# Kernel tuning notes

Hardware: AMD Instinct MI355X
Metric: run time of the kernel (lower is better)

The kernel has to match this reference:

```python
import jax, jax.numpy as jnp
import numpy as np

N_NODES = 50000
N_EDGES = 800000
N_GRAPHS = 512
VOCAB = 100000
EMB = 64
HID = 128
CLASSES = 2


def setup_inputs() -> dict:
    key = jax.random.key(0)
    ks = jax.random.split(key, 12)
    x = jax.random.randint(ks[0], (N_NODES,), 0, VOCAB)
    edge_index = jax.random.randint(ks[1], (2, N_EDGES), 0, N_NODES)
    batch = jnp.sort(jax.random.randint(ks[2], (N_NODES,), 0, N_GRAPHS))
    s = lambda fan_in: 1.0 / np.sqrt(fan_in)
    emb_table = jax.random.normal(ks[3], (VOCAB, EMB), jnp.float32)
    w1_l = jax.random.uniform(ks[4], (EMB, HID), jnp.float32, -s(EMB), s(EMB))
    b1 = jnp.zeros((HID,), jnp.float32)
    w1_r = jax.random.uniform(ks[5], (EMB, HID), jnp.float32, -s(EMB), s(EMB))
    w2_l = jax.random.uniform(ks[6], (HID, HID), jnp.float32, -s(HID), s(HID))
    b2 = jnp.zeros((HID,), jnp.float32)
    w2_r = jax.random.uniform(ks[7], (HID, HID), jnp.float32, -s(HID), s(HID))
    w_out = jax.random.uniform(ks[8], (HID, CLASSES), jnp.float32, -s(HID), s(HID))
    b_out = jnp.zeros((CLASSES,), jnp.float32)
    return {"x": x, "edge_index": edge_index, "batch": batch,
            "emb_table": emb_table, "w1_l": w1_l, "b1": b1, "w1_r": w1_r,
            "w2_l": w2_l, "b2": b2, "w2_r": w2_r, "w_out": w_out, "b_out": b_out}


def _sage_conv(h, src, dst, w_l, b_l, w_r):
    # PyG SAGEConv (mean aggr): out = lin_l(mean_{j in N(i)} x_j) + lin_r(x_i)
    msg = h[src]                                              # [E, F] gather
    agg = jax.ops.segment_sum(msg, dst, num_segments=N_NODES)  # [N, F]
    deg = jax.ops.segment_sum(jnp.ones((src.shape[0],), h.dtype), dst,
                              num_segments=N_NODES)
    mean = agg / jnp.maximum(deg, 1.0)[:, None]
    return mean @ w_l + b_l + h @ w_r


def reference(x, edge_index, batch, emb_table, w1_l, b1, w1_r,
              w2_l, b2, w2_r, w_out, b_out):
    src, dst = edge_index[0], edge_index[1]
    h = emb_table[x]                                          # [N, EMB]
    h = jax.nn.relu(_sage_conv(h, src, dst, w1_l, b1, w1_r))
    # dropout is identity in eval mode
    h = jax.nn.relu(_sage_conv(h, src, dst, w2_l, b2, w2_r))
    # global mean pool over graphs
    pooled = jax.ops.segment_sum(h, batch, num_segments=N_GRAPHS)
    cnt = jax.ops.segment_sum(jnp.ones((N_NODES,), h.dtype), batch,
                              num_segments=N_GRAPHS)
    pooled = pooled / jnp.maximum(cnt, 1.0)[:, None]
    return pooled @ w_out + b_out                              # [G, CLASSES]
```

## Files before the change

### kernel.cpp

```cpp
#include <hip/hip_runtime.h>
#include <hip/hip_bf16.h>

#define N_NODES 50000
#define N_EDGES 800000
#define N_GRAPHS 512
#define EMB 64
#define HID 128

__global__ void k_embed_hist(const int* __restrict__ x, const float* __restrict__ emb,
                             const int* __restrict__ ei, float* __restrict__ h0,
                             int* __restrict__ deg) {
    int t = blockIdx.x * 256 + threadIdx.x;
    if (t >= N_EDGES) return;
    int n = t >> 4, c4 = t & 15;
    const float4* e4 = (const float4*)emb;
    ((float4*)h0)[(size_t)n * 16 + c4] = e4[(size_t)x[n] * 16 + c4];
    atomicAdd(&deg[ei[N_EDGES + t]], 1);
}

__global__ void k_scanA(const int* __restrict__ deg, int* __restrict__ rowptr,
                        int* __restrict__ bsums) {
    __shared__ int s[256];
    int t = threadIdx.x, i = blockIdx.x * 256 + t;
    int v = (i < N_NODES) ? deg[i] : 0;
    s[t] = v; __syncthreads();
    int xv = v;
    for (int off = 1; off < 256; off <<= 1) {
        int y = (t >= off) ? s[t - off] : 0;
        __syncthreads();
        xv += y; s[t] = xv;
        __syncthreads();
    }
    if (i < N_NODES) rowptr[i] = xv - v;
    if (t == 255) bsums[blockIdx.x] = xv;
}

__global__ void k_scanB(int* __restrict__ bsums, int nb) {
    __shared__ int s[256];
    int t = threadIdx.x;
    int v = (t < nb) ? bsums[t] : 0;
    s[t] = v; __syncthreads();
    int xv = v;
    for (int off = 1; off < 256; off <<= 1) {
        int y = (t >= off) ? s[t - off] : 0;
        __syncthreads();
        xv += y; s[t] = xv;
        __syncthreads();
    }
    if (t < nb) bsums[t] = xv - v;
}

__global__ void k_scanC(int* __restrict__ rowptr, int* __restrict__ wp,
                        const int* __restrict__ bsums) {
    int i = blockIdx.x * 256 + threadIdx.x;
    if (i < N_NODES) {
        int v = rowptr[i] + bsums[blockIdx.x];
        rowptr[i] = v;
        wp[i] = v;
    }
    if (i == 0) rowptr[N_NODES] = N_EDGES;
}

__global__ void k_scatter(const int* __restrict__ ei, int* __restrict__ wp,
                          int* __restrict__ nbr) {
    int e = blockIdx.x * 256 + threadIdx.x;
    if (e >= N_EDGES) return;
    int s = ei[e], d = ei[N_EDGES + e];
    int pos = atomicAdd(&wp[d], 1);
    nbr[pos] = s;
}

template <int F>
__global__ __launch_bounds__(256) void k_agg(const float* __restrict__ h,
                                             const int* __restrict__ rowptr,
                                             const int* __restrict__ nbr,
                                             float* __restrict__ mean) {
    int w = (blockIdx.x * 256 + threadIdx.x) >> 6;
    int l = threadIdx.x & 63;
    const float4* h4 = (const float4*)h;
    float4* m4 = (float4*)mean;

    int n, c;
    if constexpr (F == 128) { n = w * 2 + (l >> 5); c = l & 31; }
    else                    { n = w * 4 + (l >> 4); c = l & 15; }
    if (n >= N_NODES) return;
    constexpr int C = F / 4;

    int r0 = rowptr[n], r1 = rowptr[n + 1];
    float inv = 1.0f / (float)max(r1 - r0, 1);

    float4 a0 = {0,0,0,0}, a1 = {0,0,0,0}, a2 = {0,0,0,0}, a3 = {0,0,0,0};
    int i = r0;
    for (; i + 3 < r1; i += 4) {
        int s0 = nbr[i], s1 = nbr[i + 1], s2 = nbr[i + 2], s3 = nbr[i + 3];
        float4 v0 = h4[(size_t)s0 * C + c];
        float4 v1 = h4[(size_t)s1 * C + c];
        float4 v2 = h4[(size_t)s2 * C + c];
        float4 v3 = h4[(size_t)s3 * C + c];
        a0.x += v0.x; a0.y += v0.y; a0.z += v0.z; a0.w += v0.w;
        a1.x += v1.x; a1.y += v1.y; a1.z += v1.z; a1.w += v1.w;
        a2.x += v2.x; a2.y += v2.y; a2.z += v2.z; a2.w += v2.w;
        a3.x += v3.x; a3.y += v3.y; a3.z += v3.z; a3.w += v3.w;
    }
    for (; i < r1; ++i) {
        float4 v = h4[(size_t)nbr[i] * C + c];
        a0.x += v.x; a0.y += v.y; a0.z += v.z; a0.w += v.w;
    }
    float4 r;
    r.x = ((a0.x + a1.x) + (a2.x + a3.x)) * inv;
    r.y = ((a0.y + a1.y) + (a2.y + a3.y)) * inv;
    r.z = ((a0.z + a1.z) + (a2.z + a3.z)) * inv;
    r.w = ((a0.w + a1.w) + (a2.w + a3.w)) * inv;
    m4[(size_t)n * C + c] = r;
}

template <int K>
__global__ __launch_bounds__(512) void k_layer(
    const float* __restrict__ hself, const float* __restrict__ hmean,
    const float* __restrict__ w_r, const float* __restrict__ w_l,
    const float* __restrict__ bias, float* __restrict__ out) {
    constexpr int LS = K + 1;
    __shared__ float ls[64 * LS];
    int base = blockIdx.x * 64;
    int t = threadIdx.x;
    int lane = t & 63;
    int wid = __builtin_amdgcn_readfirstlane(t >> 6);
    int j0 = wid * 16;
    int node = base + lane;
    bool valid = node < N_NODES;

    float acc[16];
    #pragma unroll
    for (int j = 0; j < 16; j++) acc[j] = bias[j0 + j];

    const float* lrow = &ls[lane * LS];

    {
        const float4* h4 = (const float4*)hself;
        for (int idx = t; idx < 64 * (K / 4); idx += 512) {
            int r = idx / (K / 4), c4 = idx % (K / 4);
            float4 v = (base + r < N_NODES) ? h4[(size_t)(base + r) * (K / 4) + c4]
                                            : make_float4(0.f, 0.f, 0.f, 0.f);
            float* dp = &ls[r * LS + c4 * 4];
            dp[0] = v.x; dp[1] = v.y; dp[2] = v.z; dp[3] = v.w;
        }
    }
    __syncthreads();
    #pragma unroll 4
    for (int k = 0; k < K; k++) {
        float hv = lrow[k];
        const float* wk = &w_r[(size_t)k * 128 + j0];
        #pragma unroll
        for (int j = 0; j < 16; j++) acc[j] = fmaf(hv, wk[j], acc[j]);
    }
    __syncthreads();

    {
        const float4* h4 = (const float4*)hmean;
        for (int idx = t; idx < 64 * (K / 4); idx += 512) {
            int r = idx / (K / 4), c4 = idx % (K / 4);
            float4 v = (base + r < N_NODES) ? h4[(size_t)(base + r) * (K / 4) + c4]
                                            : make_float4(0.f, 0.f, 0.f, 0.f);
            float* dp = &ls[r * LS + c4 * 4];
            dp[0] = v.x; dp[1] = v.y; dp[2] = v.z; dp[3] = v.w;
        }
    }
    __syncthreads();
    #pragma unroll 4
    for (int k = 0; k < K; k++) {
        float hv = lrow[k];
        const float* wk = &w_l[(size_t)k * 128 + j0];
        #pragma unroll
        for (int j = 0; j < 16; j++) acc[j] = fmaf(hv, wk[j], acc[j]);
    }

    if (!valid) return;
    float4* o4 = (float4*)out;
    #pragma unroll
    for (int jj = 0; jj < 4; jj++) {
        float4 v;
        v.x = fmaxf(acc[jj * 4 + 0], 0.f);
        v.y = fmaxf(acc[jj * 4 + 1], 0.f);
        v.z = fmaxf(acc[jj * 4 + 2], 0.f);
        v.w = fmaxf(acc[jj * 4 + 3], 0.f);
        o4[(size_t)node * 32 + wid * 4 + jj] = v;
    }
}

__global__ void k_pool_head(const float* __restrict__ h2, const int* __restrict__ batch,
                            const float* __restrict__ w_out, const float* __restrict__ b_out,
                            float* __restrict__ out) {
    int g = blockIdx.x;
    int lo = 0, hi = N_NODES;
    while (lo < hi) { int mid = (lo + hi) >> 1; if (batch[mid] < g) lo = mid + 1; else hi = mid; }
    int s = lo;
    lo = s; hi = N_NODES;
    while (lo < hi) { int mid = (lo + hi) >> 1; if (batch[mid] < g + 1) lo = mid + 1; else hi = mid; }
    int e = lo;

    int f = threadIdx.x & 127, half = threadIdx.x >> 7;
    float acc = 0.0f;
    for (int r = s + half; r < e; r += 2) acc += h2[(size_t)r * 128 + f];
    __shared__ float tmp[256];
    tmp[threadIdx.x] = acc;
    __syncthreads();
    if (half == 0) {
        float p = (tmp[f] + tmp[f + 128]) / (float)max(e - s, 1);
        tmp[f]       = p * w_out[f * 2 + 0];
        tmp[f + 128] = p * w_out[f * 2 + 1];
    }
    __syncthreads();
    for (int str = 64; str > 0; str >>= 1) {
        if (threadIdx.x < str) {
            tmp[threadIdx.x] += tmp[threadIdx.x + str];
            tmp[threadIdx.x + 128] += tmp[threadIdx.x + 128 + str];
        }
        __syncthreads();
    }
    if (threadIdx.x == 0) {
        out[(size_t)g * 2 + 0] = tmp[0] + b_out[0];
        out[(size_t)g * 2 + 1] = tmp[128] + b_out[1];
    }
}

extern "C" void kernel_launch(void* const* d_in, const int* in_sizes, int n_in,
                              void* d_out, int out_size, void* d_ws, size_t ws_size,
                              hipStream_t stream) {
    const int*   x      = (const int*)d_in[0];
    const int*   ei     = (const int*)d_in[1];
    const int*   batch  = (const int*)d_in[2];
    const float* emb    = (const float*)d_in[3];
    const float* w1_l   = (const float*)d_in[4];
    const float* b1     = (const float*)d_in[5];
    const float* w1_r   = (const float*)d_in[6];
    const float* w2_l   = (const float*)d_in[7];
    const float* b2     = (const float*)d_in[8];
    const float* w2_r   = (const float*)d_in[9];
    const float* w_out  = (const float*)d_in[10];
    const float* b_out  = (const float*)d_in[11];
    float* out = (float*)d_out;

    float* F = (float*)d_ws;
    float* h0    = F;
    float* mean1 = h0 + (size_t)N_NODES * 64;
    float* h1    = mean1 + (size_t)N_NODES * 64;
    float* mean2 = h1 + (size_t)N_NODES * 128;
    float* h2    = h0;
    int*   deg   = (int*)(mean2 + (size_t)N_NODES * 128);
    int*   rowptr= deg + N_NODES;
    int*   wp    = rowptr + N_NODES + 1;
    int*   nbr   = wp + N_NODES;
    int*   bsums = nbr + N_EDGES;

    const int NB = (N_NODES + 255) / 256;

    hipMemsetAsync(deg, 0, (size_t)N_NODES * sizeof(int), stream);

    k_embed_hist<<<(N_EDGES + 255) / 256, 256, 0, stream>>>(x, emb, ei, h0, deg);
    k_scanA<<<NB, 256, 0, stream>>>(deg, rowptr, bsums);
    k_scanB<<<1, 256, 0, stream>>>(bsums, NB);
    k_scanC<<<NB, 256, 0, stream>>>(rowptr, wp, bsums);
    k_scatter<<<(N_EDGES + 255) / 256, 256, 0, stream>>>(ei, wp, nbr);

    k_agg<64><<<(N_NODES + 15) / 16, 256, 0, stream>>>(h0, rowptr, nbr, mean1);
    k_layer<64><<<(N_NODES + 63) / 64, 512, 0, stream>>>(h0, mean1, w1_r, w1_l, b1, h1);

    k_agg<128><<<(N_NODES + 7) / 8, 256, 0, stream>>>(h1, rowptr, nbr, mean2);
    k_layer<128><<<(N_NODES + 63) / 64, 512, 0, stream>>>(h1, mean2, w2_r, w2_l, b2, h2);

    k_pool_head<<<N_GRAPHS, 256, 0, stream>>>(h2, batch, w_out, b_out, out);

    (void)in_sizes; (void)n_in; (void)out_size; (void)ws_size;
}
```

Measured before the change: 387.3 us.

## Fuse neighbor mean aggregation into SAGE layer kernels

Removes the separate aggregation kernels and computes each node's neighbor mean directly into shared memory inside the layer kernel, then runs the linear transform from there. This avoids writing and re-reading the mean buffers in global memory and saves two launches. The gather now runs inside 512-thread blocks that also hold the GEMM tile, which may lower occupancy and limit how well gather latency is hidden. The shared row stride is padded to K+2, and h2 gets its own buffer instead of aliasing h0.

Result: slower. 398.2 us (+2.8%).

```diff
diff --git a/kernel.cpp b/kernel.cpp
--- a/kernel.cpp
+++ b/kernel.cpp
@@ -70,56 +70,14 @@
     nbr[pos] = s;
 }
 
-template <int F>
-__global__ __launch_bounds__(256) void k_agg(const float* __restrict__ h,
-                                             const int* __restrict__ rowptr,
-                                             const int* __restrict__ nbr,
-                                             float* __restrict__ mean) {
-    int w = (blockIdx.x * 256 + threadIdx.x) >> 6;
-    int l = threadIdx.x & 63;
-    const float4* h4 = (const float4*)h;
-    float4* m4 = (float4*)mean;
-
-    int n, c;
-    if constexpr (F == 128) { n = w * 2 + (l >> 5); c = l & 31; }
-    else                    { n = w * 4 + (l >> 4); c = l & 15; }
-    if (n >= N_NODES) return;
-    constexpr int C = F / 4;
-
-    int r0 = rowptr[n], r1 = rowptr[n + 1];
-    float inv = 1.0f / (float)max(r1 - r0, 1);
-
-    float4 a0 = {0,0,0,0}, a1 = {0,0,0,0}, a2 = {0,0,0,0}, a3 = {0,0,0,0};
-    int i = r0;
-    for (; i + 3 < r1; i += 4) {
-        int s0 = nbr[i], s1 = nbr[i + 1], s2 = nbr[i + 2], s3 = nbr[i + 3];
-        float4 v0 = h4[(size_t)s0 * C + c];
-        float4 v1 = h4[(size_t)s1 * C + c];
-        float4 v2 = h4[(size_t)s2 * C + c];
-        float4 v3 = h4[(size_t)s3 * C + c];
-        a0.x += v0.x; a0.y += v0.y; a0.z += v0.z; a0.w += v0.w;
-        a1.x += v1.x; a1.y += v1.y; a1.z += v1.z; a1.w += v1.w;
-        a2.x += v2.x; a2.y += v2.y; a2.z += v2.z; a2.w += v2.w;
-        a3.x += v3.x; a3.y += v3.y; a3.z += v3.z; a3.w += v3.w;
-    }
-    for (; i < r1; ++i) {
-        float4 v = h4[(size_t)nbr[i] * C + c];
-        a0.x += v.x; a0.y += v.y; a0.z += v.z; a0.w += v.w;
-    }
-    float4 r;
-    r.x = ((a0.x + a1.x) + (a2.x + a3.x)) * inv;
-    r.y = ((a0.y + a1.y) + (a2.y + a3.y)) * inv;
-    r.z = ((a0.z + a1.z) + (a2.z + a3.z)) * inv;
-    r.w = ((a0.w + a1.w) + (a2.w + a3.w)) * inv;
-    m4[(size_t)n * C + c] = r;
-}
-
 template <int K>
-__global__ __launch_bounds__(512) void k_layer(
-    const float* __restrict__ hself, const float* __restrict__ hmean,
-    const float* __restrict__ w_r, const float* __restrict__ w_l,
-    const float* __restrict__ bias, float* __restrict__ out) {
-    constexpr int LS = K + 1;
+__global__ __launch_bounds__(512) void k_fused_layer(
+    const float* __restrict__ hin, const int* __restrict__ rowptr,
+    const int* __restrict__ nbr, const float* __restrict__ w_r,
+    const float* __restrict__ w_l, const float* __restrict__ bias,
+    float* __restrict__ out) {
+    constexpr int LS = K + 2;
+    constexpr int C4 = K / 4;
     __shared__ float ls[64 * LS];
     int base = blockIdx.x * 64;
     int t = threadIdx.x;
@@ -134,16 +92,14 @@
     for (int j = 0; j < 16; j++) acc[j] = bias[j0 + j];
 
     const float* lrow = &ls[lane * LS];
-
-    {
-        const float4* h4 = (const float4*)hself;
-        for (int idx = t; idx < 64 * (K / 4); idx += 512) {
-            int r = idx / (K / 4), c4 = idx % (K / 4);
-            float4 v = (base + r < N_NODES) ? h4[(size_t)(base + r) * (K / 4) + c4]
-                                            : make_float4(0.f, 0.f, 0.f, 0.f);
-            float* dp = &ls[r * LS + c4 * 4];
-            dp[0] = v.x; dp[1] = v.y; dp[2] = v.z; dp[3] = v.w;
-        }
+    const float4* h4 = (const float4*)hin;
+
+    for (int idx = t; idx < 64 * C4; idx += 512) {
+        int r = idx / C4, c4 = idx % C4;
+        float4 v = (base + r < N_NODES) ? h4[(size_t)(base + r) * C4 + c4]
+                                        : make_float4(0.f, 0.f, 0.f, 0.f);
+        float* dp = &ls[r * LS + c4 * 4];
+        dp[0] = v.x; dp[1] = v.y; dp[2] = v.z; dp[3] = v.w;
     }
     __syncthreads();
     #pragma unroll 4
@@ -156,16 +112,44 @@
     __syncthreads();
 
     {
-        const float4* h4 = (const float4*)hmean;
-        for (int idx = t; idx < 64 * (K / 4); idx += 512) {
-            int r = idx / (K / 4), c4 = idx % (K / 4);
-            float4 v = (base + r < N_NODES) ? h4[(size_t)(base + r) * (K / 4) + c4]
-                                            : make_float4(0.f, 0.f, 0.f, 0.f);
-            float* dp = &ls[r * LS + c4 * 4];
-            dp[0] = v.x; dp[1] = v.y; dp[2] = v.z; dp[3] = v.w;
+        constexpr int RPW = 64 / C4;
+        int sub = lane / C4;
+        int c   = lane % C4;
+        #pragma unroll
+        for (int it = 0; it < 8 / RPW; ++it) {
+            int row = wid * 8 + it * RPW + sub;
+            int n = base + row;
+            float4 a0 = {0,0,0,0}, a1 = {0,0,0,0}, a2 = {0,0,0,0}, a3 = {0,0,0,0};
+            float inv = 0.0f;
+            if (n < N_NODES) {
+                int r0 = rowptr[n], r1 = rowptr[n + 1];
+                inv = 1.0f / (float)max(r1 - r0, 1);
+                int i = r0;
+                for (; i + 3 < r1; i += 4) {
+                    int s0 = nbr[i], s1 = nbr[i + 1], s2 = nbr[i + 2], s3 = nbr[i + 3];
+                    float4 v0 = h4[(size_t)s0 * C4 + c];
+                    float4 v1 = h4[(size_t)s1 * C4 + c];
+                    float4 v2 = h4[(size_t)s2 * C4 + c];
+                    float4 v3 = h4[(size_t)s3 * C4 + c];
+                    a0.x += v0.x; a0.y += v0.y; a0.z += v0.z; a0.w += v0.w;
+                    a1.x += v1.x; a1.y += v1.y; a1.z += v1.z; a1.w += v1.w;
+                    a2.x += v2.x; a2.y += v2.y; a2.z += v2.z; a2.w += v2.w;
+                    a3.x += v3.x; a3.y += v3.y; a3.z += v3.z; a3.w += v3.w;
+                }
+                for (; i < r1; ++i) {
+                    float4 v = h4[(size_t)nbr[i] * C4 + c];
+                    a0.x += v.x; a0.y += v.y; a0.z += v.z; a0.w += v.w;
+                }
+            }
+            float* dp = &ls[row * LS + c * 4];
+            dp[0] = ((a0.x + a1.x) + (a2.x + a3.x)) * inv;
+            dp[1] = ((a0.y + a1.y) + (a2.y + a3.y)) * inv;
+            dp[2] = ((a0.z + a1.z) + (a2.z + a3.z)) * inv;
+            dp[3] = ((a0.w + a1.w) + (a2.w + a3.w)) * inv;
         }
     }
     __syncthreads();
+
     #pragma unroll 4
     for (int k = 0; k < K; k++) {
         float hv = lrow[k];
@@ -242,11 +226,9 @@
 
     float* F = (float*)d_ws;
     float* h0    = F;
-    float* mean1 = h0 + (size_t)N_NODES * 64;
-    float* h1    = mean1 + (size_t)N_NODES * 64;
-    float* mean2 = h1 + (size_t)N_NODES * 128;
-    float* h2    = h0;
-    int*   deg   = (int*)(mean2 + (size_t)N_NODES * 128);
+    float* h1    = h0 + (size_t)N_NODES * 64;
+    float* h2    = h1 + (size_t)N_NODES * 128;
+    int*   deg   = (int*)(h2 + (size_t)N_NODES * 128);
     int*   rowptr= deg + N_NODES;
     int*   wp    = rowptr + N_NODES + 1;
     int*   nbr   = wp + N_NODES;
@@ -262,11 +244,10 @@
     k_scanC<<<NB, 256, 0, stream>>>(rowptr, wp, bsums);
     k_scatter<<<(N_EDGES + 255) / 256, 256, 0, stream>>>(ei, wp, nbr);
 
-    k_agg<64><<<(N_NODES + 15) / 16, 256, 0, stream>>>(h0, rowptr, nbr, mean1);
-    k_layer<64><<<(N_NODES + 63) / 64, 512, 0, stream>>>(h0, mean1, w1_r, w1_l, b1, h1);
-
-    k_agg<128><<<(N_NODES + 7) / 8, 256, 0, stream>>>(h1, rowptr, nbr, mean2);
-    k_layer<128><<<(N_NODES + 63) / 64, 512, 0, stream>>>(h1, mean2, w2_r, w2_l, b2, h2);
+    k_fused_layer<64><<<(N_NODES + 63) / 64, 512, 0, stream>>>(
+        h0, rowptr, nbr, w1_r, w1_l, b1, h1);
+    k_fused_layer<128><<<(N_NODES + 63) / 64, 512, 0, stream>>>(
+        h1, rowptr, nbr, w2_r, w2_l, b2, h2);
 
     k_pool_head<<<N_GRAPHS, 256, 0, stream>>>(h2, batch, w_out, b_out, out);
 
```

## Transpose weights once and read node rows directly in layer GEMM

Applied to the files above, without the earlier changes.

Adds an on-device transpose of the four SAGE weight matrices, folded into the embedding/histogram kernel, so each weight output column becomes contiguous in k. The layer kernel drops its shared-memory staging and barriers: each lane reads its own node row straight from global memory in 32-wide chunks and does FMAs against wave-uniform transposed weight rows. The neighbour-aggregation loop is also unrolled from 4 to 8 independent gathers to keep more loads in flight. The trade-off is more registers per thread and uncoalesced per-lane row loads (a 256/512-byte stride between lanes) in place of the coalesced tile load into LDS.

Measured after the change: 526.5 us. 1.36x slower.

```diff
diff --git a/kernel.cpp b/kernel.cpp
--- a/kernel.cpp
+++ b/kernel.cpp
@@ -9,13 +9,30 @@
 
 __global__ void k_embed_hist(const int* __restrict__ x, const float* __restrict__ emb,
                              const int* __restrict__ ei, float* __restrict__ h0,
-                             int* __restrict__ deg) {
+                             int* __restrict__ deg,
+                             const float* __restrict__ w1r, const float* __restrict__ w1l,
+                             const float* __restrict__ w2r, const float* __restrict__ w2l,
+                             float* __restrict__ wt1r, float* __restrict__ wt1l,
+                             float* __restrict__ wt2r, float* __restrict__ wt2l) {
     int t = blockIdx.x * 256 + threadIdx.x;
     if (t >= N_EDGES) return;
     int n = t >> 4, c4 = t & 15;
     const float4* e4 = (const float4*)emb;
     ((float4*)h0)[(size_t)n * 16 + c4] = e4[(size_t)x[n] * 16 + c4];
     atomicAdd(&deg[ei[N_EDGES + t]], 1);
+    if (t < 8192) {
+        int j = t & 127, k = t >> 7;
+        wt1r[j * 64 + k] = w1r[k * 128 + j];
+    } else if (t < 16384) {
+        int u = t - 8192; int j = u & 127, k = u >> 7;
+        wt1l[j * 64 + k] = w1l[k * 128 + j];
+    } else if (t < 32768) {
+        int u = t - 16384; int j = u & 127, k = u >> 7;
+        wt2r[j * 128 + k] = w2r[k * 128 + j];
+    } else if (t < 49152) {
+        int u = t - 32768; int j = u & 127, k = u >> 7;
+        wt2l[j * 128 + k] = w2l[k * 128 + j];
+    }
 }
 
 __global__ void k_scanA(const int* __restrict__ deg, int* __restrict__ rowptr,
@@ -89,90 +106,97 @@
     int r0 = rowptr[n], r1 = rowptr[n + 1];
     float inv = 1.0f / (float)max(r1 - r0, 1);
 
-    float4 a0 = {0,0,0,0}, a1 = {0,0,0,0}, a2 = {0,0,0,0}, a3 = {0,0,0,0};
+    float4 a[8];
+    #pragma unroll
+    for (int u = 0; u < 8; ++u) a[u] = make_float4(0.f, 0.f, 0.f, 0.f);
+
     int i = r0;
-    for (; i + 3 < r1; i += 4) {
-        int s0 = nbr[i], s1 = nbr[i + 1], s2 = nbr[i + 2], s3 = nbr[i + 3];
+    for (; i + 7 < r1; i += 8) {
+        int s0 = nbr[i + 0], s1 = nbr[i + 1], s2 = nbr[i + 2], s3 = nbr[i + 3];
+        int s4 = nbr[i + 4], s5 = nbr[i + 5], s6 = nbr[i + 6], s7 = nbr[i + 7];
         float4 v0 = h4[(size_t)s0 * C + c];
         float4 v1 = h4[(size_t)s1 * C + c];
         float4 v2 = h4[(size_t)s2 * C + c];
         float4 v3 = h4[(size_t)s3 * C + c];
-        a0.x += v0.x; a0.y += v0.y; a0.z += v0.z; a0.w += v0.w;
-        a1.x += v1.x; a1.y += v1.y; a1.z += v1.z; a1.w += v1.w;
-        a2.x += v2.x; a2.y += v2.y; a2.z += v2.z; a2.w += v2.w;
-        a3.x += v3.x; a3.y += v3.y; a3.z += v3.z; a3.w += v3.w;
+        float4 v4 = h4[(size_t)s4 * C + c];
+        float4 v5 = h4[(size_t)s5 * C + c];
+        float4 v6 = h4[(size_t)s6 * C + c];
+        float4 v7 = h4[(size_t)s7 * C + c];
+        a[0].x += v0.x; a[0].y += v0.y; a[0].z += v0.z; a[0].w += v0.w;
+        a[1].x += v1.x; a[1].y += v1.y; a[1].z += v1.z; a[1].w += v1.w;
+        a[2].x += v2.x; a[2].y += v2.y; a[2].z += v2.z; a[2].w += v2.w;
+        a[3].x += v3.x; a[3].y += v3.y; a[3].z += v3.z; a[3].w += v3.w;
+        a[4].x += v4.x; a[4].y += v4.y; a[4].z += v4.z; a[4].w += v4.w;
+        a[5].x += v5.x; a[5].y += v5.y; a[5].z += v5.z; a[5].w += v5.w;
+        a[6].x += v6.x; a[6].y += v6.y; a[6].z += v6.z; a[6].w += v6.w;
+        a[7].x += v7.x; a[7].y += v7.y; a[7].z += v7.z; a[7].w += v7.w;
+    }
+    for (; i + 3 < r1; i += 4) {
+        int s0 = nbr[i + 0], s1 = nbr[i + 1], s2 = nbr[i + 2], s3 = nbr[i + 3];
+        float4 v0 = h4[(size_t)s0 * C + c];
+        float4 v1 = h4[(size_t)s1 * C + c];
+        float4 v2 = h4[(size_t)s2 * C + c];
+        float4 v3 = h4[(size_t)s3 * C + c];
+        a[0].x += v0.x; a[0].y += v0.y; a[0].z += v0.z; a[0].w += v0.w;
+        a[1].x += v1.x; a[1].y += v1.y; a[1].z += v1.z; a[1].w += v1.w;
+        a[2].x += v2.x; a[2].y += v2.y; a[2].z += v2.z; a[2].w += v2.w;
+        a[3].x += v3.x; a[3].y += v3.y; a[3].z += v3.z; a[3].w += v3.w;
     }
     for (; i < r1; ++i) {
         float4 v = h4[(size_t)nbr[i] * C + c];
-        a0.x += v.x; a0.y += v.y; a0.z += v.z; a0.w += v.w;
-    }
-    float4 r;
-    r.x = ((a0.x + a1.x) + (a2.x + a3.x)) * inv;
-    r.y = ((a0.y + a1.y) + (a2.y + a3.y)) * inv;
-    r.z = ((a0.z + a1.z) + (a2.z + a3.z)) * inv;
-    r.w = ((a0.w + a1.w) + (a2.w + a3.w)) * inv;
-    m4[(size_t)n * C + c] = r;
+        a[0].x += v.x; a[0].y += v.y; a[0].z += v.z; a[0].w += v.w;
+    }
+    #pragma unroll
+    for (int u = 1; u < 8; ++u) {
+        a[0].x += a[u].x; a[0].y += a[u].y; a[0].z += a[u].z; a[0].w += a[u].w;
+    }
+    m4[(size_t)n * C + c] = make_float4(a[0].x * inv, a[0].y * inv,
+                                        a[0].z * inv, a[0].w * inv);
+}
+
+template <int K>
+__device__ __forceinline__ void gemm_pass(const float4* __restrict__ src,
+                                          const float* __restrict__ wt,
+                                          int nclamp, int j0, float (&acc)[16]) {
+    const float4* rp = src + (size_t)nclamp * (K / 4);
+    for (int kc = 0; kc < K / 32; ++kc) {
+        float4 r4[8];
+        #pragma unroll
+        for (int cc = 0; cc < 8; ++cc) r4[cc] = rp[kc * 8 + cc];
+        float row[32];
+        #pragma unroll
+        for (int cc = 0; cc < 8; ++cc) {
+            row[cc * 4 + 0] = r4[cc].x; row[cc * 4 + 1] = r4[cc].y;
+            row[cc * 4 + 2] = r4[cc].z; row[cc * 4 + 3] = r4[cc].w;
+        }
+        #pragma unroll
+        for (int j = 0; j < 16; ++j) {
+            const float* wr = wt + (size_t)(j0 + j) * K + kc * 32;
+            #pragma unroll
+            for (int k = 0; k < 32; ++k) acc[j] = fmaf(row[k], wr[k], acc[j]);
+        }
+    }
 }
 
 template <int K>
 __global__ __launch_bounds__(512) void k_layer(
     const float* __restrict__ hself, const float* __restrict__ hmean,
-    const float* __restrict__ w_r, const float* __restrict__ w_l,
+    const float* __restrict__ wt_r, const float* __restrict__ wt_l,
     const float* __restrict__ bias, float* __restrict__ out) {
-    constexpr int LS = K + 1;
-    __shared__ float ls[64 * LS];
-    int base = blockIdx.x * 64;
     int t = threadIdx.x;
     int lane = t & 63;
     int wid = __builtin_amdgcn_readfirstlane(t >> 6);
     int j0 = wid * 16;
-    int node = base + lane;
+    int node = blockIdx.x * 64 + lane;
     bool valid = node < N_NODES;
+    int nclamp = valid ? node : N_NODES - 1;
 
     float acc[16];
     #pragma unroll
     for (int j = 0; j < 16; j++) acc[j] = bias[j0 + j];
 
-    const float* lrow = &ls[lane * LS];
-
-    {
-        const float4* h4 = (const float4*)hself;
-        for (int idx = t; idx < 64 * (K / 4); idx += 512) {
-            int r = idx / (K / 4), c4 = idx % (K / 4);
-            float4 v = (base + r < N_NODES) ? h4[(size_t)(base + r) * (K / 4) + c4]
-                                            : make_float4(0.f, 0.f, 0.f, 0.f);
-            float* dp = &ls[r * LS + c4 * 4];
-            dp[0] = v.x; dp[1] = v.y; dp[2] = v.z; dp[3] = v.w;
-        }
-    }
-    __syncthreads();
-    #pragma unroll 4
-    for (int k = 0; k < K; k++) {
-        float hv = lrow[k];
-        const float* wk = &w_r[(size_t)k * 128 + j0];
-        #pragma unroll
-        for (int j = 0; j < 16; j++) acc[j] = fmaf(hv, wk[j], acc[j]);
-    }
-    __syncthreads();
-
-    {
-        const float4* h4 = (const float4*)hmean;
-        for (int idx = t; idx < 64 * (K / 4); idx += 512) {
-            int r = idx / (K / 4), c4 = idx % (K / 4);
-            float4 v = (base + r < N_NODES) ? h4[(size_t)(base + r) * (K / 4) + c4]
-                                            : make_float4(0.f, 0.f, 0.f, 0.f);
-            float* dp = &ls[r * LS + c4 * 4];
-            dp[0] = v.x; dp[1] = v.y; dp[2] = v.z; dp[3] = v.w;
-        }
-    }
-    __syncthreads();
-    #pragma unroll 4
-    for (int k = 0; k < K; k++) {
-        float hv = lrow[k];
-        const float* wk = &w_l[(size_t)k * 128 + j0];
-        #pragma unroll
-        for (int j = 0; j < 16; j++) acc[j] = fmaf(hv, wk[j], acc[j]);
-    }
+    gemm_pass<K>((const float4*)hself, wt_r, nclamp, j0, acc);
+    gemm_pass<K>((const float4*)hmean, wt_l, nclamp, j0, acc);
 
     if (!valid) return;
     float4* o4 = (float4*)out;
@@ -251,22 +275,27 @@
     int*   wp    = rowptr + N_NODES + 1;
     int*   nbr   = wp + N_NODES;
     int*   bsums = nbr + N_EDGES;
+    float* wt1r  = (float*)(bsums + 256);
+    float* wt1l  = wt1r + 128 * 64;
+    float* wt2r  = wt1l + 128 * 64;
+    float* wt2l  = wt2r + 128 * 128;
 
     const int NB = (N_NODES + 255) / 256;
 
     hipMemsetAsync(deg, 0, (size_t)N_NODES * sizeof(int), stream);
 
-    k_embed_hist<<<(N_EDGES + 255) / 256, 256, 0, stream>>>(x, emb, ei, h0, deg);
+    k_embed_hist<<<(N_EDGES + 255) / 256, 256, 0, stream>>>(
+        x, emb, ei, h0, deg, w1_r, w1_l, w2_r, w2_l, wt1r, wt1l, wt2r, wt2l);
     k_scanA<<<NB, 256, 0, stream>>>(deg, rowptr, bsums);
     k_scanB<<<1, 256, 0, stream>>>(bsums, NB);
     k_scanC<<<NB, 256, 0, stream>>>(rowptr, wp, bsums);
     k_scatter<<<(N_EDGES + 255) / 256, 256, 0, stream>>>(ei, wp, nbr);
 
     k_agg<64><<<(N_NODES + 15) / 16, 256, 0, stream>>>(h0, rowptr, nbr, mean1);
-    k_layer<64><<<(N_NODES + 63) / 64, 512, 0, stream>>>(h0, mean1, w1_r, w1_l, b1, h1);
+    k_layer<64><<<(N_NODES + 63) / 64, 512, 0, stream>>>(h0, mean1, wt1r, wt1l, b1, h1);
 
     k_agg<128><<<(N_NODES + 7) / 8, 256, 0, stream>>>(h1, rowptr, nbr, mean2);
-    k_layer<128><<<(N_NODES + 63) / 64, 512, 0, stream>>>(h1, mean2, w2_r, w2_l, b2, h2);
+    k_layer<128><<<(N_NODES + 63) / 64, 512, 0, stream>>>(h1, mean2, wt2r, wt2l, b2, h2);
 
     k_pool_head<<<N_GRAPHS, 256, 0, stream>>>(h2, batch, w_out, b_out, out);
 
```
